# Kernel tuning notes

Hardware: AMD Instinct MI355X
Metric: run time of the kernel (lower is better)

The kernel has to match this reference:

```python
import jax, jax.numpy as jnp
import numpy as np

B, T, D = 4, 2048, 1024
NF = 512
NB = 4
FREQ_SCALE = 0.1


def _w(k, shape, scale):
    return jax.random.normal(k, shape, jnp.float32) * scale


def setup_inputs() -> dict:
    key = jax.random.key(0)
    ks = jax.random.split(key, 16)
    d = D ** -0.5
    inp = {}
    inp['x'] = jax.random.normal(ks[0], (B, T, D), jnp.float32)
    inp['norm_g'] = jnp.ones((D,), jnp.float32)
    inp['norm_b'] = jnp.zeros((D,), jnp.float32)
    inp['Wconcept'] = _w(ks[1], (D, D), d); inp['bconcept'] = jnp.zeros((D,), jnp.float32)
    inp['Wcg'] = _w(ks[2], (D, D), d); inp['bcg'] = jnp.zeros((D,), jnp.float32)
    inp['Wfg'] = _w(ks[3], (NF, D), d); inp['bfg'] = jnp.zeros((NF,), jnp.float32)
    inp['Wtg'] = _w(ks[4], (1, D), d); inp['btg'] = jnp.zeros((1,), jnp.float32)
    inp['Wband'] = _w(ks[5], (NB, D), d); inp['bband'] = jnp.zeros((NB,), jnp.float32)
    inp['Wsp'] = _w(ks[6], (2 * NF, D), d)  # to_spectral, no bias
    inp['freq_importance'] = jnp.ones((NF,), jnp.float32)
    inp['log_decay'] = (jnp.linspace(-3.0, -0.001, NF) + _w(ks[7], (NF,), 0.1)).astype(jnp.float32)
    inp['frequencies'] = ((jnp.arange(NF, dtype=jnp.float32) / NF * 2.0 - 1.0) * 0.2)
    inp['dt'] = jnp.ones((NF,), jnp.float32) * 0.5
    inp['Wgate'] = _w(ks[8], (D, D), d); inp['bgate'] = jnp.zeros((D,), jnp.float32)
    inp['Wfs'] = _w(ks[9], (D, 2 * NF), (2 * NF) ** -0.5)  # from_spectral, no bias
    inp['output_scale'] = jnp.ones((1,), jnp.float32) * 0.5
    inp['norm2_g'] = jnp.ones((D,), jnp.float32)
    inp['norm2_b'] = jnp.zeros((D,), jnp.float32)
    inp['W1'] = _w(ks[10], (4 * D, D), d); inp['b1'] = jnp.zeros((4 * D,), jnp.float32)
    inp['W2'] = _w(ks[11], (D, 4 * D), (4 * D) ** -0.5); inp['b2'] = jnp.zeros((D,), jnp.float32)
    return inp


def _ln(x, g, b):
    m = jnp.mean(x, axis=-1, keepdims=True)
    v = jnp.var(x, axis=-1, keepdims=True)
    return (x - m) * jax.lax.rsqrt(v + 1e-5) * g + b


def reference(x, norm_g, norm_b, Wconcept, bconcept, Wcg, bcg, Wfg, bfg, Wtg, btg,
              Wband, bband, Wsp, freq_importance, log_decay, frequencies, dt,
              Wgate, bgate, Wfs, output_scale, norm2_g, norm2_b, W1, b1, W2, b2):
    b_, t_, _ = x.shape
    nf = log_decay.shape[0]
    nb = Wband.shape[0]
    residual = x
    xn = _ln(x, norm_g, norm_b)

    concept = xn @ Wconcept.T + bconcept
    concept_preserved = concept * jax.nn.sigmoid(xn @ Wcg.T + bcg)

    forget_gates = jax.nn.sigmoid(xn @ Wfg.T + bfg)          # (B,T,NF)
    temporal_strength = jax.nn.sigmoid(xn @ Wtg.T + btg)     # (B,T,1)
    band_strengths = jax.nn.sigmoid(xn @ Wband.T + bband)    # (B,T,NB)

    sp = xn @ Wsp.T                                          # (B,T,2*NF)
    u = jax.lax.complex(sp[..., :nf], sp[..., nf:]) * forget_gates

    decay = jax.nn.sigmoid(log_decay) * (jax.nn.softmax(freq_importance) * nf)
    omega = frequencies * FREQ_SCALE * (jax.nn.sigmoid(dt) * 2.0)
    rot = jax.lax.complex(jnp.cos(omega), jnp.sin(omega))    # (NF,)
    A = decay * rot                                          # (NF,) complex

    band_scale = jnp.repeat(band_strengths, nf // nb, axis=-1)  # (B,T,NF)
    A_exp = A * band_scale                                   # (B,T,NF) complex

    ones_first = jnp.ones((b_, 1, nf), A_exp.dtype)
    powers = jnp.cumprod(jnp.concatenate([ones_first, A_exp[:, :-1, :]], axis=1), axis=1)
    powers = powers * temporal_strength
    kernel = powers * rot

    n_fft = 2 * t_
    Uf = jnp.fft.fft(u, n=n_fft, axis=1)
    Kf = jnp.fft.fft(kernel, n=n_fft, axis=1)
    y = jnp.fft.ifft(Uf * Kf, n=n_fft, axis=1)[:, :t_, :]

    spectral_out = jnp.concatenate([y.real, y.imag], axis=-1)
    y_proj = (spectral_out @ Wfs.T) * output_scale
    gate_values = jax.nn.sigmoid(xn @ Wgate.T + bgate)
    y_gated = (y_proj * gate_values + concept_preserved) / 2.0  # dropout: eval mode

    x2 = residual + y_gated
    xn2 = _ln(x2, norm2_g, norm2_b)
    h = jax.nn.gelu(xn2 @ W1.T + b1, approximate=False)
    return x2 + h @ W2.T + b2
```

## Files before the change

### kernel.cpp

```cpp
#include <hip/hip_runtime.h>
#include <hip/hip_bf16.h>
#include <cstdint>
#include <cstddef>

typedef unsigned short u16;
typedef unsigned int u32;
typedef short bf16x8 __attribute__((ext_vector_type(8)));
typedef float f32x4 __attribute__((ext_vector_type(4)));
typedef float f32x2 __attribute__((ext_vector_type(2)));

static constexpr int Bb = 4, Tt = 2048, Dd = 1024, NFf = 512, NBb = 4;
static constexpr int Mm = Bb * Tt;
static constexpr int NZz = 4736;
static constexpr int Lc = 32;

#define DEV __device__ __forceinline__

typedef const __attribute__((address_space(1))) u32* gas_p;
typedef __attribute__((address_space(3))) u32* las_p;

DEV u16 f2bf(float f) {
    uint32_t u = __float_as_uint(f);
    u = (u + 0x7FFF + ((u >> 16) & 1)) >> 16;
    return (u16)u;
}
DEV float bf2f(u16 h) { return __uint_as_float(((uint32_t)h) << 16); }
DEV float sigm(float x) { return 1.0f / (1.0f + __expf(-x)); }
DEV float gelu_ex(float t) { return 0.5f * t * (1.0f + erff(t * 0.70710678118f)); }

static constexpr int NW0 = NZz * Dd;
static constexpr int NW1 = Dd * 2 * NFf;
static constexpr int NW2 = 4 * Dd * Dd;
static constexpr int NW3 = 4 * Dd * Dd;
static constexpr int NWTOT = NW0 + NW1 + NW2 + NW3;

__global__ __launch_bounds__(256) void prep_all(
    const float* __restrict__ Wconcept, const float* __restrict__ Wcg,
    const float* __restrict__ Wfg, const float* __restrict__ Wgate,
    const float* __restrict__ Wsp, const float* __restrict__ Wtg,
    const float* __restrict__ Wband,
    const float* __restrict__ bconcept, const float* __restrict__ bcg,
    const float* __restrict__ bfg, const float* __restrict__ bgate,
    const float* __restrict__ btg, const float* __restrict__ bband,
    const float* __restrict__ Wfs, const float* __restrict__ W1,
    const float* __restrict__ W2,
    const float* __restrict__ fi, const float* __restrict__ logd,
    const float* __restrict__ freqs, const float* __restrict__ dtv,
    u16* __restrict__ wcat, float* __restrict__ bias_cat,
    u16* __restrict__ wfs, u16* __restrict__ w1b, u16* __restrict__ w2b,
    float* __restrict__ rr, float* __restrict__ ri,
    float* __restrict__ Ar, float* __restrict__ Ai)
{
    if (blockIdx.x == 0) {
        __shared__ float red[256];
        int t = threadIdx.x;
        float v0 = fi[t], v1 = fi[t + 256];
        red[t] = fmaxf(v0, v1); __syncthreads();
        for (int s = 128; s; s >>= 1) { if (t < s) red[t] = fmaxf(red[t], red[t + s]); __syncthreads(); }
        float mx = red[0]; __syncthreads();
        float e0 = expf(v0 - mx), e1 = expf(v1 - mx);
        red[t] = e0 + e1; __syncthreads();
        for (int s = 128; s; s >>= 1) { if (t < s) red[t] += red[t + s]; __syncthreads(); }
        float inv = 1.0f / red[0];
#pragma unroll
        for (int k = 0; k < 2; k++) {
            int f = t + k * 256;
            float e = k ? e1 : e0;
            float decay = sigm(logd[f]) * (e * inv * (float)NFf);
            float omega = freqs[f] * 0.1f * (sigm(dtv[f]) * 2.0f);
            float cc = cosf(omega), ss = sinf(omega);
            rr[f] = cc; ri[f] = ss; Ar[f] = decay * cc; Ai[f] = decay * ss;
        }
        return;
    }
    int i = (blockIdx.x - 1) * 256 + threadIdx.x;
    if (i < NW0) {
        int r = i >> 10, c = i & 1023;
        float v;
        if      (r < 1024) v = Wconcept[r * 1024 + c];
        else if (r < 2048) v = Wcg[(r - 1024) * 1024 + c];
        else if (r < 2560) v = Wfg[(r - 2048) * 1024 + c];
        else if (r < 3584) v = Wgate[(r - 2560) * 1024 + c];
        else if (r < 4608) v = Wsp[(r - 3584) * 1024 + c];
        else if (r == 4608) v = Wtg[c];
        else if (r < 4613) v = Wband[(r - 4609) * 1024 + c];
        else v = 0.0f;
        wcat[i] = f2bf(v);
        if (c == 0) {
            float bv;
            if      (r < 1024) bv = bconcept[r];
            else if (r < 2048) bv = bcg[r - 1024];
            else if (r < 2560) bv = bfg[r - 2048];
            else if (r < 3584) bv = bgate[r - 2560];
            else if (r < 4608) bv = 0.0f;
            else if (r == 4608) bv = btg[0];
            else if (r < 4613) bv = bband[r - 4609];
            else bv = 0.0f;
            bias_cat[r] = bv;
        }
    } else if (i < NW0 + NW1) {
        int j = i - NW0; wfs[j] = f2bf(Wfs[j]);
    } else if (i < NW0 + NW1 + NW2) {
        int j = i - NW0 - NW1; w1b[j] = f2bf(W1[j]);
    } else {
        int j = i - NW0 - NW1 - NW2; w2b[j] = f2bf(W2[j]);
    }
}

__global__ __launch_bounds__(256) void ln_kernel(
    const float* __restrict__ x, const float* __restrict__ g,
    const float* __restrict__ b, u16* __restrict__ out_bf)
{
    const int m = blockIdx.x, tid = threadIdx.x;
    float4 v = ((const float4*)(x + (size_t)m * Dd))[tid];
    float s1 = v.x + v.y + v.z + v.w;
    float s2 = v.x * v.x + v.y * v.y + v.z * v.z + v.w * v.w;
    __shared__ float lds[16];
    for (int o = 32; o; o >>= 1) { s1 += __shfl_down(s1, o); s2 += __shfl_down(s2, o); }
    int lane = tid & 63, w = tid >> 6;
    if (!lane) { lds[w] = s1; lds[8 + w] = s2; }
    __syncthreads();
    s1 = lds[0] + lds[1] + lds[2] + lds[3];
    s2 = lds[8] + lds[9] + lds[10] + lds[11];
    float mean = s1 * (1.0f / Dd);
    float var  = s2 * (1.0f / Dd) - mean * mean;
    float rstd = rsqrtf(var + 1e-5f);
    float4 gv = ((const float4*)g)[tid];
    float4 bv = ((const float4*)b)[tid];
    ushort4 o;
    o.x = f2bf((v.x - mean) * rstd * gv.x + bv.x);
    o.y = f2bf((v.y - mean) * rstd * gv.y + bv.y);
    o.z = f2bf((v.z - mean) * rstd * gv.z + bv.z);
    o.w = f2bf((v.w - mean) * rstd * gv.w + bv.w);
    ((ushort4*)(out_bf + (size_t)m * Dd))[tid] = o;
}

template<int MODE>
__global__ __launch_bounds__(256, 2) void gemm_bt(
    const u16* __restrict__ A, const u16* __restrict__ Bw,
    const float* __restrict__ bias, const float* __restrict__ add,
    void* __restrict__ Cout, int M, int N, int K)
{
    __shared__ __align__(16) u16 smA[128 * 32];
    __shared__ __align__(16) u16 smB[128 * 32];
    const int tid = threadIdx.x;
    const int m0 = blockIdx.x * 128;
    const int n0 = blockIdx.y * 128;
    const int w = tid >> 6, lane = tid & 63;
    const int wr = w >> 1, wc = w & 1;
    const int quad = lane >> 4, l16 = lane & 15;

    const int r0 = tid >> 2;
    const int cs = (tid & 3) ^ ((tid >> 3) & 3);
    const u16* gA0 = A + (size_t)(m0 + r0) * K + cs * 8;
    const u16* gA1 = gA0 + (size_t)64 * K;
    const u16* gB0 = Bw + (size_t)(n0 + r0) * K + cs * 8;
    const u16* gB1 = gB0 + (size_t)64 * K;
    las_p lA0 = (las_p)(smA + tid * 8);
    las_p lA1 = (las_p)(smA + 2048 + tid * 8);
    las_p lB0 = (las_p)(smB + tid * 8);
    las_p lB1 = (las_p)(smB + 2048 + tid * 8);

    const int swz = (l16 >> 1) & 3;
    const int sA = (quad ^ swz) * 8;

    f32x4 acc[4][4];
#pragma unroll
    for (int i = 0; i < 4; i++)
#pragma unroll
        for (int j = 0; j < 4; j++) acc[i][j] = {0.f, 0.f, 0.f, 0.f};

    for (int k0 = 0; k0 < K; k0 += 32) {
        __syncthreads();
        __builtin_amdgcn_global_load_lds((gas_p)(gA0 + k0), lA0, 16, 0, 0);
        __builtin_amdgcn_global_load_lds((gas_p)(gA1 + k0), lA1, 16, 0, 0);
        __builtin_amdgcn_global_load_lds((gas_p)(gB0 + k0), lB0, 16, 0, 0);
        __builtin_amdgcn_global_load_lds((gas_p)(gB1 + k0), lB1, 16, 0, 0);
        __syncthreads();
        bf16x8 af[4], bfv[4];
#pragma unroll
        for (int mi = 0; mi < 4; mi++)
            af[mi] = *(const bf16x8*)&smA[(wr * 64 + mi * 16 + l16) * 32 + sA];
#pragma unroll
        for (int ni = 0; ni < 4; ni++)
            bfv[ni] = *(const bf16x8*)&smB[(wc * 64 + ni * 16 + l16) * 32 + sA];
#pragma unroll
        for (int mi = 0; mi < 4; mi++)
#pragma unroll
            for (int ni = 0; ni < 4; ni++)
                acc[mi][ni] = __builtin_amdgcn_mfma_f32_16x16x32_bf16(
                    af[mi], bfv[ni], acc[mi][ni], 0, 0, 0);
    }

#pragma unroll
    for (int mi = 0; mi < 4; mi++) {
#pragma unroll
        for (int ni = 0; ni < 4; ni++) {
            const int gn = n0 + wc * 64 + ni * 16 + l16;
            const int gm0 = m0 + wr * 64 + mi * 16 + quad * 4;
            if constexpr (MODE == 0 || MODE == 2 || MODE == 4) {
                float bv = (MODE == 4) ? 0.0f : bias[gn];
                float t0 = acc[mi][ni][0] + bv, t1 = acc[mi][ni][1] + bv;
                float t2 = acc[mi][ni][2] + bv, t3 = acc[mi][ni][3] + bv;
                if constexpr (MODE == 2) {
                    t0 = gelu_ex(t0); t1 = gelu_ex(t1); t2 = gelu_ex(t2); t3 = gelu_ex(t3);
                }
                __hip_bfloat162 h01 = __float22bfloat162_rn(float2{t0, t1});
                __hip_bfloat162 h23 = __float22bfloat162_rn(float2{t2, t3});
                __hip_bfloat16* o = (__hip_bfloat16*)Cout;
                o[(size_t)(gm0 + 0) * N + gn] = h01.x;
                o[(size_t)(gm0 + 1) * N + gn] = h01.y;
                o[(size_t)(gm0 + 2) * N + gn] = h23.x;
                o[(size_t)(gm0 + 3) * N + gn] = h23.y;
            } else {
#pragma unroll
                for (int r = 0; r < 4; r++) {
                    const int gm = gm0 + r;
                    float v = acc[mi][ni][r];
                    if constexpr (MODE == 1) {
                        ((float*)Cout)[(size_t)gm * N + gn] = v;
                    } else {
                        ((float*)Cout)[(size_t)gm * N + gn] = v + bias[gn] + add[(size_t)gm * N + gn];
                    }
                }
            }
        }
    }
}

__global__ __launch_bounds__(256) void prepA_kernel(
    const u16* __restrict__ Z, f32x2* __restrict__ u2,
    float* __restrict__ ts, float* __restrict__ bs)
{
    int i = blockIdx.x * 256 + threadIdx.x;
    if (i >= Mm * NFf) return;
    int m = i >> 9, f = i & (NFf - 1);
    const u16* zr = Z + (size_t)m * NZz;
    float fg  = sigm(bf2f(zr[2048 + f]));
    float spr = bf2f(zr[3584 + f]);
    float spi = bf2f(zr[3584 + NFf + f]);
    u2[i] = f32x2{spr * fg, spi * fg};
    if (f == 0) {
        ts[m] = sigm(bf2f(zr[4608]));
#pragma unroll
        for (int j = 0; j < NBb; j++) bs[m * NBb + j] = sigm(bf2f(zr[4609 + j]));
    }
}

__global__ __launch_bounds__(256) void makek_kernel(
    const float* __restrict__ Ar, const float* __restrict__ Ai,
    const float* __restrict__ rr, const float* __restrict__ ri,
    const float* __restrict__ ts, const float* __restrict__ bs,
    f32x2* __restrict__ k2)
{
    int g = blockIdx.x * 256 + threadIdx.x;
    if (g >= Bb * NFf) return;
    int b = g >> 9, f = g & (NFf - 1);
    float Pr = 1.0f, Pi = 0.0f;
    float ar = Ar[f], ai = Ai[f], cr = rr[f], ci = ri[f];
    const int band = f >> 7;
    for (int tau = 0; tau < Lc; tau++) {
        float tsv = ts[b * Tt + tau];
        k2[((size_t)b * Lc + tau) * NFf + f] = f32x2{tsv * (cr * Pr - ci * Pi),
                                                     tsv * (cr * Pi + ci * Pr)};
        float bsv = bs[(b * Tt + tau) * NBb + band];
        float er = ar * bsv, ei = ai * bsv;
        float nPr = Pr * er - Pi * ei;
        float nPi = Pr * ei + Pi * er;
        Pr = nPr; Pi = nPi;
    }
}

__global__ __launch_bounds__(256) void conv_kernel(
    const f32x2* __restrict__ u2, const f32x2* __restrict__ k2,
    u16* __restrict__ spec)
{
    __shared__ f32x2 su[96 * 64];
    __shared__ f32x2 sk[Lc * 64];
    const int tid = threadIdx.x;
    const int fl = tid & 63;
    const int ty = tid >> 6;
    const int f0 = blockIdx.x * 64;
    const int t0 = blockIdx.y * 64;
    const int b  = blockIdx.z;

    for (int i = tid; i < Lc * 64; i += 256) {
        int tau = i >> 6, ff = i & 63;
        sk[i] = k2[((size_t)b * Lc + tau) * NFf + f0 + ff];
    }
    for (int i = tid; i < 96 * 64; i += 256) {
        int r = i >> 6, ff = i & 63;
        int t = t0 - 32 + r;
        f32x2 v = {0.f, 0.f};
        if (t >= 0) v = u2[((size_t)b * Tt + t) * NFf + f0 + ff];
        su[i] = v;
    }
    __syncthreads();

    f32x2 y[16];
#pragma unroll
    for (int j = 0; j < 16; j++) y[j] = f32x2{0.f, 0.f};
    const int tl0 = 32 + ty * 16;
    for (int tau = 0; tau < Lc; tau++) {
        f32x2 k = sk[tau * 64 + fl];
#pragma unroll
        for (int j = 0; j < 16; j++) {
            f32x2 u = su[(tl0 + j - tau) * 64 + fl];
            y[j].x += u.x * k.x - u.y * k.y;
            y[j].y += u.x * k.y + u.y * k.x;
        }
    }
#pragma unroll
    for (int j = 0; j < 16; j++) {
        size_t row = (size_t)(b * Tt + t0 + ty * 16 + j);
        spec[row * (2 * NFf) + f0 + fl]       = f2bf(y[j].x);
        spec[row * (2 * NFf) + NFf + f0 + fl] = f2bf(y[j].y);
    }
}

__global__ __launch_bounds__(256) void fuse2_ln_kernel(
    const float* __restrict__ x, const u16* __restrict__ Z,
    const u16* __restrict__ P2, const float* __restrict__ osc,
    const float* __restrict__ g2, const float* __restrict__ b2v,
    float* __restrict__ x2, u16* __restrict__ xn2)
{
    const int m = blockIdx.x, tid = threadIdx.x;
    const float os = osc[0];
    const u16* zr = Z + (size_t)m * NZz;
    float4 xv = ((const float4*)(x + (size_t)m * Dd))[tid];
    ushort4 pv = ((const ushort4*)(P2 + (size_t)m * Dd))[tid];
    float vals[4]; float s1 = 0.0f, s2 = 0.0f;
#pragma unroll
    for (int j = 0; j < 4; j++) {
        int d = tid * 4 + j;
        float concept = bf2f(zr[d]);
        float cg   = sigm(bf2f(zr[1024 + d]));
        float gate = sigm(bf2f(zr[2560 + d]));
        float p = bf2f((&pv.x)[j]);
        float v = (&xv.x)[j] + 0.5f * (p * os * gate + concept * cg);
        vals[j] = v; s1 += v; s2 += v * v;
    }
    __shared__ float lds[16];
    for (int o = 32; o; o >>= 1) { s1 += __shfl_down(s1, o); s2 += __shfl_down(s2, o); }
    int lane = tid & 63, w = tid >> 6;
    if (!lane) { lds[w] = s1; lds[8 + w] = s2; }
    __syncthreads();
    s1 = lds[0] + lds[1] + lds[2] + lds[3];
    s2 = lds[8] + lds[9] + lds[10] + lds[11];
    float mean = s1 * (1.0f / Dd);
    float var  = s2 * (1.0f / Dd) - mean * mean;
    float rstd = rsqrtf(var + 1e-5f);
    float4 xo; ushort4 no;
#pragma unroll
    for (int j = 0; j < 4; j++) {
        int d = tid * 4 + j;
        (&xo.x)[j] = vals[j];
        (&no.x)[j] = f2bf((vals[j] - mean) * rstd * g2[d] + b2v[d]);
    }
    ((float4*)(x2 + (size_t)m * Dd))[tid] = xo;
    ((ushort4*)(xn2 + (size_t)m * Dd))[tid] = no;
}

extern "C" void kernel_launch(void* const* d_in, const int* in_sizes, int n_in,
                              void* d_out, int out_size, void* d_ws, size_t ws_size,
                              hipStream_t stream)
{
    const float* x        = (const float*)d_in[0];
    const float* norm_g   = (const float*)d_in[1];
    const float* norm_b   = (const float*)d_in[2];
    const float* Wconcept = (const float*)d_in[3];
    const float* bconcept = (const float*)d_in[4];
    const float* Wcg      = (const float*)d_in[5];
    const float* bcg      = (const float*)d_in[6];
    const float* Wfg      = (const float*)d_in[7];
    const float* bfg      = (const float*)d_in[8];
    const float* Wtg      = (const float*)d_in[9];
    const float* btg      = (const float*)d_in[10];
    const float* Wband    = (const float*)d_in[11];
    const float* bband    = (const float*)d_in[12];
    const float* Wsp      = (const float*)d_in[13];
    const float* fi       = (const float*)d_in[14];
    const float* logd     = (const float*)d_in[15];
    const float* freqs    = (const float*)d_in[16];
    const float* dtv      = (const float*)d_in[17];
    const float* Wgate    = (const float*)d_in[18];
    const float* bgate    = (const float*)d_in[19];
    const float* Wfs      = (const float*)d_in[20];
    const float* osc      = (const float*)d_in[21];
    const float* n2g      = (const float*)d_in[22];
    const float* n2b      = (const float*)d_in[23];
    const float* W1       = (const float*)d_in[24];
    const float* b1       = (const float*)d_in[25];
    const float* W2       = (const float*)d_in[26];
    const float* b2       = (const float*)d_in[27];

    char* ws = (char*)d_ws;
    size_t off = 0;
    auto alloc = [&](size_t bytes) { size_t c = off; off += (bytes + 255) & ~(size_t)255; return c; };
    size_t o_wcat = alloc((size_t)NZz * Dd * 2);
    size_t o_bias = alloc((size_t)NZz * 4);
    size_t o_wfs  = alloc((size_t)Dd * 2 * NFf * 2);
    size_t o_w1   = alloc((size_t)4 * Dd * Dd * 2);
    size_t o_w2   = alloc((size_t)4 * Dd * Dd * 2);
    size_t o_xn   = alloc((size_t)Mm * Dd * 2);
    size_t o_Z    = alloc((size_t)Mm * NZz * 2);
    size_t o_u    = alloc((size_t)Mm * NFf * 8);
    size_t o_spec = alloc((size_t)Mm * Dd * 2);
    size_t o_P2   = alloc((size_t)Mm * Dd * 2);
    size_t o_k2   = alloc((size_t)Bb * Lc * NFf * 8);
    size_t o_rr   = alloc(NFf * 4);
    size_t o_ri   = alloc(NFf * 4);
    size_t o_Ar   = alloc(NFf * 4);
    size_t o_Ai   = alloc(NFf * 4);
    size_t o_ts   = alloc(Mm * 4);
    size_t o_bs   = alloc((size_t)Mm * NBb * 4);
    if (ws_size < off) return;

    u16*   wcat = (u16*)(ws + o_wcat);
    float* bias = (float*)(ws + o_bias);
    u16*   wfs  = (u16*)(ws + o_wfs);
    u16*   w1b  = (u16*)(ws + o_w1);
    u16*   w2b  = (u16*)(ws + o_w2);
    u16*   xn   = (u16*)(ws + o_xn);
    u16*   Zb   = (u16*)(ws + o_Z);
    u16*   hb   = (u16*)(ws + o_Z);
    f32x2* u2   = (f32x2*)(ws + o_u);
    float* x2   = (float*)(ws + o_u);
    u16*   spec = (u16*)(ws + o_spec);
    u16*   xn2  = (u16*)(ws + o_spec);
    u16*   P2   = (u16*)(ws + o_P2);
    f32x2* k2   = (f32x2*)(ws + o_k2);
    float* rr   = (float*)(ws + o_rr);
    float* ri   = (float*)(ws + o_ri);
    float* Ar   = (float*)(ws + o_Ar);
    float* Ai   = (float*)(ws + o_Ai);
    float* ts   = (float*)(ws + o_ts);
    float* bs   = (float*)(ws + o_bs);

    prep_all<<<1 + NWTOT / 256, 256, 0, stream>>>(
        Wconcept, Wcg, Wfg, Wgate, Wsp, Wtg, Wband,
        bconcept, bcg, bfg, bgate, btg, bband,
        Wfs, W1, W2, fi, logd, freqs, dtv,
        wcat, bias, wfs, w1b, w2b, rr, ri, Ar, Ai);

    ln_kernel<<<Mm, 256, 0, stream>>>(x, norm_g, norm_b, xn);

    gemm_bt<0><<<dim3(Mm / 128, NZz / 128), 256, 0, stream>>>(
        xn, wcat, bias, nullptr, (void*)Zb, Mm, NZz, Dd);

    prepA_kernel<<<(Mm * NFf + 255) / 256, 256, 0, stream>>>(Zb, u2, ts, bs);
    makek_kernel<<<(Bb * NFf + 255) / 256, 256, 0, stream>>>(Ar, Ai, rr, ri, ts, bs, k2);

    conv_kernel<<<dim3(NFf / 64, Tt / 64, Bb), 256, 0, stream>>>(u2, k2, spec);

    gemm_bt<4><<<dim3(Mm / 128, Dd / 128), 256, 0, stream>>>(
        spec, wfs, nullptr, nullptr, (void*)P2, Mm, Dd, 2 * NFf);

    fuse2_ln_kernel<<<Mm, 256, 0, stream>>>(x, Zb, P2, osc, n2g, n2b, x2, xn2);

    gemm_bt<2><<<dim3(Mm / 128, (4 * Dd) / 128), 256, 0, stream>>>(
        xn2, w1b, b1, nullptr, (void*)hb, Mm, 4 * Dd, Dd);
    gemm_bt<3><<<dim3(Mm / 128, Dd / 128), 256, 0, stream>>>(
        hb, w2b, b2, x2, d_out, Mm, Dd, 4 * Dd);
}
```

Baseline: 577.1 us.

## Fuse LN into prep, merge prepA/makek, store intermediates in bf16, raise GEMM occupancy

Folds the first layernorm into the weight-prep launch and merges the spectral-input prep with kernel construction, which reads the gate sigmoids straight from Z and drops the ts/bs buffers. The u intermediate and the x2 residual are now stored as bf16 instead of fp32, cutting memory traffic in the conv and final GEMM epilogue. GEMM launch bounds ask for 4 blocks per SM instead of 2, which may force register spills. Keeping the residual and the conv input in bf16 loses precision.

```diff
diff --git a/kernel.cpp b/kernel.cpp
--- a/kernel.cpp
+++ b/kernel.cpp
@@ -33,6 +33,7 @@
 static constexpr int NW2 = 4 * Dd * Dd;
 static constexpr int NW3 = 4 * Dd * Dd;
 static constexpr int NWTOT = NW0 + NW1 + NW2 + NW3;
+static constexpr int NWB = NWTOT / 256;
 
 __global__ __launch_bounds__(256) void prep_all(
     const float* __restrict__ Wconcept, const float* __restrict__ Wcg,
@@ -46,12 +47,16 @@
     const float* __restrict__ W2,
     const float* __restrict__ fi, const float* __restrict__ logd,
     const float* __restrict__ freqs, const float* __restrict__ dtv,
+    const float* __restrict__ x, const float* __restrict__ norm_g,
+    const float* __restrict__ norm_b,
     u16* __restrict__ wcat, float* __restrict__ bias_cat,
     u16* __restrict__ wfs, u16* __restrict__ w1b, u16* __restrict__ w2b,
     float* __restrict__ rr, float* __restrict__ ri,
-    float* __restrict__ Ar, float* __restrict__ Ai)
-{
-    if (blockIdx.x == 0) {
+    float* __restrict__ Ar, float* __restrict__ Ai,
+    u16* __restrict__ xn)
+{
+    const int bx = blockIdx.x;
+    if (bx == 0) {
         __shared__ float red[256];
         int t = threadIdx.x;
         float v0 = fi[t], v1 = fi[t + 256];
@@ -73,45 +78,42 @@
         }
         return;
     }
-    int i = (blockIdx.x - 1) * 256 + threadIdx.x;
-    if (i < NW0) {
-        int r = i >> 10, c = i & 1023;
-        float v;
-        if      (r < 1024) v = Wconcept[r * 1024 + c];
-        else if (r < 2048) v = Wcg[(r - 1024) * 1024 + c];
-        else if (r < 2560) v = Wfg[(r - 2048) * 1024 + c];
-        else if (r < 3584) v = Wgate[(r - 2560) * 1024 + c];
-        else if (r < 4608) v = Wsp[(r - 3584) * 1024 + c];
-        else if (r == 4608) v = Wtg[c];
-        else if (r < 4613) v = Wband[(r - 4609) * 1024 + c];
-        else v = 0.0f;
-        wcat[i] = f2bf(v);
-        if (c == 0) {
-            float bv;
-            if      (r < 1024) bv = bconcept[r];
-            else if (r < 2048) bv = bcg[r - 1024];
-            else if (r < 2560) bv = bfg[r - 2048];
-            else if (r < 3584) bv = bgate[r - 2560];
-            else if (r < 4608) bv = 0.0f;
-            else if (r == 4608) bv = btg[0];
-            else if (r < 4613) bv = bband[r - 4609];
-            else bv = 0.0f;
-            bias_cat[r] = bv;
+    if (bx <= NWB) {
+        int i = (bx - 1) * 256 + threadIdx.x;
+        if (i < NW0) {
+            int r = i >> 10, c = i & 1023;
+            float v;
+            if      (r < 1024) v = Wconcept[r * 1024 + c];
+            else if (r < 2048) v = Wcg[(r - 1024) * 1024 + c];
+            else if (r < 2560) v = Wfg[(r - 2048) * 1024 + c];
+            else if (r < 3584) v = Wgate[(r - 2560) * 1024 + c];
+            else if (r < 4608) v = Wsp[(r - 3584) * 1024 + c];
+            else if (r == 4608) v = Wtg[c];
+            else if (r < 4613) v = Wband[(r - 4609) * 1024 + c];
+            else v = 0.0f;
+            wcat[i] = f2bf(v);
+            if (c == 0) {
+                float bv;
+                if      (r < 1024) bv = bconcept[r];
+                else if (r < 2048) bv = bcg[r - 1024];
+                else if (r < 2560) bv = bfg[r - 2048];
+                else if (r < 3584) bv = bgate[r - 2560];
+                else if (r < 4608) bv = 0.0f;
+                else if (r == 4608) bv = btg[0];
+                else if (r < 4613) bv = bband[r - 4609];
+                else bv = 0.0f;
+                bias_cat[r] = bv;
+            }
+        } else if (i < NW0 + NW1) {
+            int j = i - NW0; wfs[j] = f2bf(Wfs[j]);
+        } else if (i < NW0 + NW1 + NW2) {
+            int j = i - NW0 - NW1; w1b[j] = f2bf(W1[j]);
+        } else {
+            int j = i - NW0 - NW1 - NW2; w2b[j] = f2bf(W2[j]);
         }
-    } else if (i < NW0 + NW1) {
-        int j = i - NW0; wfs[j] = f2bf(Wfs[j]);
-    } else if (i < NW0 + NW1 + NW2) {
-        int j = i - NW0 - NW1; w1b[j] = f2bf(W1[j]);
-    } else {
-        int j = i - NW0 - NW1 - NW2; w2b[j] = f2bf(W2[j]);
-    }
-}
-
-__global__ __launch_bounds__(256) void ln_kernel(
-    const float* __restrict__ x, const float* __restrict__ g,
-    const float* __restrict__ b, u16* __restrict__ out_bf)
-{
-    const int m = blockIdx.x, tid = threadIdx.x;
+        return;
+    }
+    const int m = bx - NWB - 1, tid = threadIdx.x;
     float4 v = ((const float4*)(x + (size_t)m * Dd))[tid];
     float s1 = v.x + v.y + v.z + v.w;
     float s2 = v.x * v.x + v.y * v.y + v.z * v.z + v.w * v.w;
@@ -125,20 +127,20 @@
     float mean = s1 * (1.0f / Dd);
     float var  = s2 * (1.0f / Dd) - mean * mean;
     float rstd = rsqrtf(var + 1e-5f);
-    float4 gv = ((const float4*)g)[tid];
-    float4 bv = ((const float4*)b)[tid];
+    float4 gv = ((const float4*)norm_g)[tid];
+    float4 bv = ((const float4*)norm_b)[tid];
     ushort4 o;
     o.x = f2bf((v.x - mean) * rstd * gv.x + bv.x);
     o.y = f2bf((v.y - mean) * rstd * gv.y + bv.y);
     o.z = f2bf((v.z - mean) * rstd * gv.z + bv.z);
     o.w = f2bf((v.w - mean) * rstd * gv.w + bv.w);
-    ((ushort4*)(out_bf + (size_t)m * Dd))[tid] = o;
+    ((ushort4*)(xn + (size_t)m * Dd))[tid] = o;
 }
 
 template<int MODE>
-__global__ __launch_bounds__(256, 2) void gemm_bt(
+__global__ __launch_bounds__(256, 4) void gemm_bt(
     const u16* __restrict__ A, const u16* __restrict__ Bw,
-    const float* __restrict__ bias, const float* __restrict__ add,
+    const float* __restrict__ bias, const u16* __restrict__ addb,
     void* __restrict__ Cout, int M, int N, int K)
 {
     __shared__ __align__(16) u16 smA[128 * 32];
@@ -216,54 +218,45 @@
 #pragma unroll
                 for (int r = 0; r < 4; r++) {
                     const int gm = gm0 + r;
-                    float v = acc[mi][ni][r];
-                    if constexpr (MODE == 1) {
-                        ((float*)Cout)[(size_t)gm * N + gn] = v;
-                    } else {
-                        ((float*)Cout)[(size_t)gm * N + gn] = v + bias[gn] + add[(size_t)gm * N + gn];
-                    }
+                    ((float*)Cout)[(size_t)gm * N + gn] =
+                        acc[mi][ni][r] + bias[gn] + bf2f(addb[(size_t)gm * N + gn]);
                 }
             }
         }
     }
 }
 
-__global__ __launch_bounds__(256) void prepA_kernel(
-    const u16* __restrict__ Z, f32x2* __restrict__ u2,
-    float* __restrict__ ts, float* __restrict__ bs)
-{
-    int i = blockIdx.x * 256 + threadIdx.x;
-    if (i >= Mm * NFf) return;
-    int m = i >> 9, f = i & (NFf - 1);
-    const u16* zr = Z + (size_t)m * NZz;
-    float fg  = sigm(bf2f(zr[2048 + f]));
-    float spr = bf2f(zr[3584 + f]);
-    float spi = bf2f(zr[3584 + NFf + f]);
-    u2[i] = f32x2{spr * fg, spi * fg};
-    if (f == 0) {
-        ts[m] = sigm(bf2f(zr[4608]));
-#pragma unroll
-        for (int j = 0; j < NBb; j++) bs[m * NBb + j] = sigm(bf2f(zr[4609 + j]));
-    }
-}
-
-__global__ __launch_bounds__(256) void makek_kernel(
+static constexpr int NBLK_A = (Mm * NFf) / 256;
+
+__global__ __launch_bounds__(256) void prepAk_kernel(
+    const u16* __restrict__ Z, ushort2* __restrict__ u2b,
     const float* __restrict__ Ar, const float* __restrict__ Ai,
     const float* __restrict__ rr, const float* __restrict__ ri,
-    const float* __restrict__ ts, const float* __restrict__ bs,
     f32x2* __restrict__ k2)
 {
-    int g = blockIdx.x * 256 + threadIdx.x;
-    if (g >= Bb * NFf) return;
+    const int bx = blockIdx.x;
+    if (bx < NBLK_A) {
+        int i = bx * 256 + threadIdx.x;
+        int m = i >> 9, f = i & (NFf - 1);
+        const u16* zr = Z + (size_t)m * NZz;
+        float fg  = sigm(bf2f(zr[2048 + f]));
+        float spr = bf2f(zr[3584 + f]);
+        float spi = bf2f(zr[3584 + NFf + f]);
+        u2b[i] = ushort2{f2bf(spr * fg), f2bf(spi * fg)};
+        return;
+    }
+    int g = (bx - NBLK_A) * 256 + threadIdx.x;
     int b = g >> 9, f = g & (NFf - 1);
     float Pr = 1.0f, Pi = 0.0f;
     float ar = Ar[f], ai = Ai[f], cr = rr[f], ci = ri[f];
     const int band = f >> 7;
+    const u16* zb = Z + (size_t)(b * Tt) * NZz;
     for (int tau = 0; tau < Lc; tau++) {
-        float tsv = ts[b * Tt + tau];
+        const u16* zrow = zb + (size_t)tau * NZz;
+        float tsv = sigm(bf2f(zrow[4608]));
         k2[((size_t)b * Lc + tau) * NFf + f] = f32x2{tsv * (cr * Pr - ci * Pi),
                                                      tsv * (cr * Pi + ci * Pr)};
-        float bsv = bs[(b * Tt + tau) * NBb + band];
+        float bsv = sigm(bf2f(zrow[4609 + band]));
         float er = ar * bsv, ei = ai * bsv;
         float nPr = Pr * er - Pi * ei;
         float nPi = Pr * ei + Pi * er;
@@ -272,7 +265,7 @@
 }
 
 __global__ __launch_bounds__(256) void conv_kernel(
-    const f32x2* __restrict__ u2, const f32x2* __restrict__ k2,
+    const ushort2* __restrict__ u2b, const f32x2* __restrict__ k2,
     u16* __restrict__ spec)
 {
     __shared__ f32x2 su[96 * 64];
@@ -292,7 +285,10 @@
         int r = i >> 6, ff = i & 63;
         int t = t0 - 32 + r;
         f32x2 v = {0.f, 0.f};
-        if (t >= 0) v = u2[((size_t)b * Tt + t) * NFf + f0 + ff];
+        if (t >= 0) {
+            ushort2 h = u2b[((size_t)b * Tt + t) * NFf + f0 + ff];
+            v = f32x2{bf2f(h.x), bf2f(h.y)};
+        }
         su[i] = v;
     }
     __syncthreads();
@@ -322,7 +318,7 @@
     const float* __restrict__ x, const u16* __restrict__ Z,
     const u16* __restrict__ P2, const float* __restrict__ osc,
     const float* __restrict__ g2, const float* __restrict__ b2v,
-    float* __restrict__ x2, u16* __restrict__ xn2)
+    u16* __restrict__ x2b, u16* __restrict__ xn2)
 {
     const int m = blockIdx.x, tid = threadIdx.x;
     const float os = osc[0];
@@ -350,14 +346,14 @@
     float mean = s1 * (1.0f / Dd);
     float var  = s2 * (1.0f / Dd) - mean * mean;
     float rstd = rsqrtf(var + 1e-5f);
-    float4 xo; ushort4 no;
+    ushort4 xo, no;
 #pragma unroll
     for (int j = 0; j < 4; j++) {
         int d = tid * 4 + j;
-        (&xo.x)[j] = vals[j];
+        (&xo.x)[j] = f2bf(vals[j]);
         (&no.x)[j] = f2bf((vals[j] - mean) * rstd * g2[d] + b2v[d]);
     }
-    ((float4*)(x2 + (size_t)m * Dd))[tid] = xo;
+    ((ushort4*)(x2b + (size_t)m * Dd))[tid] = xo;
     ((ushort4*)(xn2 + (size_t)m * Dd))[tid] = no;
 }
 
@@ -404,7 +400,7 @@
     size_t o_w2   = alloc((size_t)4 * Dd * Dd * 2);
     size_t o_xn   = alloc((size_t)Mm * Dd * 2);
     size_t o_Z    = alloc((size_t)Mm * NZz * 2);
-    size_t o_u    = alloc((size_t)Mm * NFf * 8);
+    size_t o_u    = alloc((size_t)Mm * NFf * 4);
     size_t o_spec = alloc((size_t)Mm * Dd * 2);
     size_t o_P2   = alloc((size_t)Mm * Dd * 2);
     size_t o_k2   = alloc((size_t)Bb * Lc * NFf * 8);
@@ -412,54 +408,49 @@
     size_t o_ri   = alloc(NFf * 4);
     size_t o_Ar   = alloc(NFf * 4);
     size_t o_Ai   = alloc(NFf * 4);
-    size_t o_ts   = alloc(Mm * 4);
-    size_t o_bs   = alloc((size_t)Mm * NBb * 4);
     if (ws_size < off) return;
 
-    u16*   wcat = (u16*)(ws + o_wcat);
-    float* bias = (float*)(ws + o_bias);
-    u16*   wfs  = (u16*)(ws + o_wfs);
-    u16*   w1b  = (u16*)(ws + o_w1);
-    u16*   w2b  = (u16*)(ws + o_w2);
-    u16*   xn   = (u16*)(ws + o_xn);
-    u16*   Zb   = (u16*)(ws + o_Z);
-    u16*   hb   = (u16*)(ws + o_Z);
-    f32x2* u2   = (f32x2*)(ws + o_u);
-    float* x2   = (float*)(ws + o_u);
-    u16*   spec = (u16*)(ws + o_spec);
-    u16*   xn2  = (u16*)(ws + o_spec);
-    u16*   P2   = (u16*)(ws + o_P2);
-    f32x2* k2   = (f32x2*)(ws + o_k2);
-    float* rr   = (float*)(ws + o_rr);
-    float* ri   = (float*)(ws + o_ri);
-    float* Ar   = (float*)(ws + o_Ar);
-    float* Ai   = (float*)(ws + o_Ai);
-    float* ts   = (float*)(ws + o_ts);
-    float* bs   = (float*)(ws + o_bs);
-
-    prep_all<<<1 + NWTOT / 256, 256, 0, stream>>>(
+    u16*    wcat = (u16*)(ws + o_wcat);
+    float*  bias = (float*)(ws + o_bias);
+    u16*    wfs  = (u16*)(ws + o_wfs);
+    u16*    w1b  = (u16*)(ws + o_w1);
+    u16*    w2b  = (u16*)(ws + o_w2);
+    u16*    xn   = (u16*)(ws + o_xn);
+    u16*    Zb   = (u16*)(ws + o_Z);
+    u16*    hb   = (u16*)(ws + o_Z);
+    ushort2* u2b = (ushort2*)(ws + o_u);
+    u16*    x2b  = (u16*)(ws + o_u);
+    u16*    spec = (u16*)(ws + o_spec);
+    u16*    xn2  = (u16*)(ws + o_spec);
+    u16*    P2   = (u16*)(ws + o_P2);
+    f32x2*  k2   = (f32x2*)(ws + o_k2);
+    float*  rr   = (float*)(ws + o_rr);
+    float*  ri   = (float*)(ws + o_ri);
+    float*  Ar   = (float*)(ws + o_Ar);
+    float*  Ai   = (float*)(ws + o_Ai);
+
+    prep_all<<<1 + NWB + Mm, 256, 0, stream>>>(
         Wconcept, Wcg, Wfg, Wgate, Wsp, Wtg, Wband,
         bconcept, bcg, bfg, bgate, btg, bband,
         Wfs, W1, W2, fi, logd, freqs, dtv,
-        wcat, bias, wfs, w1b, w2b, rr, ri, Ar, Ai);
-
-    ln_kernel<<<Mm, 256, 0, stream>>>(x, norm_g, norm_b, xn);
+        x, norm_g, norm_b,
+        wcat, bias, wfs, w1b, w2b, rr, ri, Ar, Ai, xn);
 
     gemm_bt<0><<<dim3(Mm / 128, NZz / 128), 256, 0, stream>>>(
         xn, wcat, bias, nullptr, (void*)Zb, Mm, NZz, Dd);
 
-    prepA_kernel<<<(Mm * NFf + 255) / 256, 256, 0, stream>>>(Zb, u2, ts, bs);
-    makek_kernel<<<(Bb * NFf + 255) / 256, 256, 0, stream>>>(Ar, Ai, rr, ri, ts, bs, k2);
-
-    conv_kernel<<<dim3(NFf / 64, Tt / 64, Bb), 256, 0, stream>>>(u2, k2, spec);
+    prepAk_kernel<<<NBLK_A + (Bb * NFf) / 256, 256, 0, stream>>>(
+        Zb, u2b, Ar, Ai, rr, ri, k2);
+
+    conv_kernel<<<dim3(NFf / 64, Tt / 64, Bb), 256, 0, stream>>>(u2b, k2, spec);
 
     gemm_bt<4><<<dim3(Mm / 128, Dd / 128), 256, 0, stream>>>(
         spec, wfs, nullptr, nullptr, (void*)P2, Mm, Dd, 2 * NFf);
 
-    fuse2_ln_kernel<<<Mm, 256, 0, stream>>>(x, Zb, P2, osc, n2g, n2b, x2, xn2);
+    fuse2_ln_kernel<<<Mm, 256, 0, stream>>>(x, Zb, P2, osc, n2g, n2b, x2b, xn2);
 
     gemm_bt<2><<<dim3(Mm / 128, (4 * Dd) / 128), 256, 0, stream>>>(
         xn2, w1b, b1, nullptr, (void*)hb, Mm, 4 * Dd, Dd);
     gemm_bt<3><<<dim3(Mm / 128, Dd / 128), 256, 0, stream>>>(
-        hb, w2b, b2, x2, d_out, Mm, Dd, 4 * Dd);
-}
+        hb, w2b, b2, x2b, d_out, Mm, Dd, 4 * Dd);
+}
```

After: 570.6 us. No clear change (-1.1%).
